# Kernel tuning notes

Hardware: AMD Instinct MI355X
Metric: run time of the kernel (lower is better)

## Reference

```python
import jax, jax.numpy as jnp
import numpy as np
from jax import lax

B, P, NB, NF, NC, R = 128, 2048, 2000, 250, 16, 128
LS = NB - NF  # number of simulated bins = len_bins_gensig - 1


def setup_inputs() -> dict:
    key = jax.random.key(0)
    ks = jax.random.split(key, 10)
    return {
        'batched_stim_spat': jax.random.normal(ks[0], (B, P), jnp.float32),
        'stim_time': jax.random.normal(ks[1], (NB,), jnp.float32),
        'batched_initial_spike_section': (jax.random.uniform(ks[2], (B, NF)) < 0.05).astype(jnp.float32),
        'batched_coupling_cells': (jax.random.uniform(ks[3], (B, NC, NB)) < 0.05).astype(jnp.float32),
        'spatial_filter': jax.random.normal(ks[4], (P,), jnp.float32) * 0.02,
        'spatial_bias': jnp.float32(-2.0),
        'stim_timecourse_filter': jax.random.normal(ks[5], (NF,), jnp.float32) * 0.1,
        'feedback_filter': jax.random.normal(ks[6], (NF,), jnp.float32) * 0.05 - 0.02,
        'coupling_filter': jax.random.normal(ks[7], (NC, NF), jnp.float32) * 0.05,
        'u': jax.random.uniform(ks[8], (LS, B, R), jnp.float32),
        'n_repeats': R,
    }


def _corr1d_valid(x, k):
    # torch F.conv1d is cross-correlation; lax conv is too (no kernel flip)
    # x: (n,), k: (m,) -> (n - m + 1,)
    out = lax.conv_general_dilated(x[None, None, :], k[None, None, :], (1,), 'VALID',
                                   dimension_numbers=('NCH', 'OIH', 'NCH'))
    return out[0, 0]


def reference(batched_stim_spat, stim_time, batched_initial_spike_section,
              batched_coupling_cells, spatial_filter, spatial_bias,
              stim_timecourse_filter, feedback_filter, coupling_filter, u, n_repeats):
    nf = stim_timecourse_filter.shape[0]

    # stimulus time component: (n_bins - nf + 1,)
    filt_time = _corr1d_valid(stim_time, stim_timecourse_filter)

    # spatial exp arg for separable linear-spatial GLM:
    # einsum('bpt,p->bt', stim_spat[:,:,None]*filt_time, spatial_filter)
    # factors into outer product of (stim_spat @ spatial_filter) and filt_time
    stim_gensig = (batched_stim_spat @ spatial_filter)[:, None] * filt_time[None, :] + spatial_bias  # (B, T)

    # coupling exp arg: conv1d over all coupled cells -> (B, T)
    coup = lax.conv_general_dilated(batched_coupling_cells, coupling_filter[None, :, :], (1,), 'VALID',
                                    dimension_numbers=('NCH', 'OIH', 'NCH'))[:, 0, :]

    gensig_piece = stim_gensig + coup  # (B, T) with T = n_bins - nf + 1
    len_sim = gensig_piece.shape[1] - 1

    # initial feedback window: last nf spike bins, broadcast over repeats
    batch = batched_stim_spat.shape[0]
    w0 = jnp.broadcast_to(batched_initial_spike_section[:, None, :], (batch, n_repeats, nf)) + 0.0

    def step(window, xs):
        g_t, u_t = xs  # (B,), (B, R)
        fb = jnp.einsum('brk,k->br', window, feedback_filter)
        g = g_t[:, None] + fb
        spike = (u_t < jax.nn.sigmoid(g)).astype(window.dtype)  # Bernoulli(sigmoid(g))
        window = jnp.concatenate([window[:, :, 1:], spike[:, :, None]], axis=2)
        return window, spike

    xs = (jnp.swapaxes(gensig_piece[:, :len_sim], 0, 1), u[:len_sim])  # ((LS,B), (LS,B,R))
    _, spikes = lax.scan(step, w0, xs)  # spikes: (LS, B, R)

    out = jnp.concatenate([w0, jnp.moveaxis(spikes, 0, 2)], axis=2)  # (B, R, n_bins)
    return out
```

## Files before the change

kernel.cpp:

```cpp
#include <hip/hip_runtime.h>
#include <math.h>

#define B_  128
#define P_  2048
#define NB_ 2000
#define NF_ 250
#define NC_ 16
#define R_  128
#define LS_ 1750
#define NT_ 1751
#define BR_ (B_ * R_)
#define H_  16
#define NBLK_ 110

typedef int v4i __attribute__((ext_vector_type(4)));

template <int CTRL>
__device__ __forceinline__ long long dpp64i(long long x) {
    int lo = (int)x, hi = (int)(x >> 32);
    lo = __builtin_amdgcn_mov_dpp(lo, CTRL, 0xF, 0xF, true);
    hi = __builtin_amdgcn_mov_dpp(hi, CTRL, 0xF, 0xF, true);
    return ((long long)(unsigned)lo) | ((long long)hi << 32);
}

__device__ __forceinline__ double logit_fast(float uf) {
    double u = (double)uf;
    double v = 1.0 - u;
    double qd = u / v;
    long long bits = __double_as_longlong(qd);
    int e = (int)((bits >> 52) & 0x7FF) - 1023;
    double m = __longlong_as_double((bits & 0xFFFFFFFFFFFFFLL) | 0x3FF0000000000000LL);
    if (m > 1.4142135623730951) { m *= 0.5; e += 1; }
    double s = (m - 1.0) / (m + 1.0);
    double z = s * s;
    double Q = fma(z, fma(z, fma(z, fma(z, fma(z, fma(z,
        0.06666666666666667, 0.07692307692307693), 0.09090909090909091),
        0.1111111111111111), 0.14285714285714285), 0.2), 0.3333333333333333);
    double logm = fma(2.0 * s, z * Q, 2.0 * s);
    return fma((double)e, 0.6931471805599453, logm);
}

__device__ __forceinline__ long long thrq_of(double lu, double fb) {
    double thr = lu - fb;
    thr = fmin(fmax(thr, -8.0), 8.0);
    double d = fma(thr, 0x1p45, 0x1.8p52);
    return (__double_as_longlong(d) & 0xFFFFFFFFFFFFFLL) - (1LL << 51);
}

__global__ __launch_bounds__(256) void k_pre(const float* __restrict__ st,
                                             const float* __restrict__ stf,
                                             const float* __restrict__ sp,
                                             const float* __restrict__ sf,
                                             double* __restrict__ ft,
                                             double* __restrict__ sdot) {
    if (blockIdx.x < 7) {
        int t = blockIdx.x * 256 + threadIdx.x;
        if (t >= NT_) return;
        double s = 0.0;
        for (int k = 0; k < NF_; ++k) s += (double)st[t + k] * (double)stf[k];
        ft[t] = s;
    } else {
        __shared__ double red[256];
        int b = blockIdx.x - 7;
        double s = 0.0;
        for (int p = threadIdx.x; p < P_; p += 256)
            s += (double)sp[(size_t)b * P_ + p] * (double)sf[p];
        red[threadIdx.x] = s;
        __syncthreads();
        for (int off = 128; off > 0; off >>= 1) {
            if (threadIdx.x < off) red[threadIdx.x] += red[threadIdx.x + off];
            __syncthreads();
        }
        if (threadIdx.x == 0) sdot[b] = red[0];
    }
}

__global__ __launch_bounds__(256) void k_coup(const float* __restrict__ cc,
                                              const float* __restrict__ cf,
                                              const double* __restrict__ sdot,
                                              const double* __restrict__ ft,
                                              const float* __restrict__ bias,
                                              double* __restrict__ gensig) {
    __shared__ __align__(16) float  ccs[NC_ * 512];
    __shared__ __align__(16) double cfs[NC_ * 256];
    __shared__ double red[3][64][4];
    int b = blockIdx.y, t0 = blockIdx.x * 256;
    int tid = threadIdx.x, lane = tid & 63, wv = tid >> 6;

    for (int idx = tid; idx < NC_ * 128; idx += 256) {
        int c = idx >> 7, j4 = (idx & 127) * 4, src = t0 + j4;
        const float* p = cc + ((size_t)b * NC_ + c) * NB_ + src;
        float4 v;
        if (src + 3 < NB_) v = *(const float4*)p;
        else {
            v.x = (src     < NB_) ? p[0] : 0.f;
            v.y = (src + 1 < NB_) ? p[1] : 0.f;
            v.z = (src + 2 < NB_) ? p[2] : 0.f;
            v.w = (src + 3 < NB_) ? p[3] : 0.f;
        }
        *(float4*)&ccs[c * 512 + j4] = v;
    }
    for (int idx = tid; idx < NC_ * 256; idx += 256) {
        int c = idx >> 8, k = idx & 255;
        cfs[idx] = (k < NF_) ? (double)cf[c * NF_ + k] : 0.0;
    }
    __syncthreads();

    double a0 = 0, a1 = 0, a2 = 0, a3 = 0;
    int base = lane * 4;
    for (int c = wv; c < NC_; c += 4) {
        const float*  row  = &ccs[c * 512];
        const double* crow = &cfs[c * 256];
        float4 cur = *(const float4*)&row[base];
        for (int k4 = 0; k4 < 252; k4 += 4) {
            float4 nxt = *(const float4*)&row[base + k4 + 4];
            double e0 = cur.x, e1 = cur.y, e2 = cur.z, e3 = cur.w;
            double e4 = nxt.x, e5 = nxt.y, e6 = nxt.z;
            double c0 = crow[k4], c1 = crow[k4 + 1], c2 = crow[k4 + 2], c3 = crow[k4 + 3];
            a0 += e0 * c0 + e1 * c1 + e2 * c2 + e3 * c3;
            a1 += e1 * c0 + e2 * c1 + e3 * c2 + e4 * c3;
            a2 += e2 * c0 + e3 * c1 + e4 * c2 + e5 * c3;
            a3 += e3 * c0 + e4 * c1 + e5 * c2 + e6 * c3;
            cur = nxt;
        }
    }
    if (wv > 0) {
        red[wv - 1][lane][0] = a0; red[wv - 1][lane][1] = a1;
        red[wv - 1][lane][2] = a2; red[wv - 1][lane][3] = a3;
    }
    __syncthreads();
    if (wv == 0) {
        a0 += red[0][lane][0] + red[1][lane][0] + red[2][lane][0];
        a1 += red[0][lane][1] + red[1][lane][1] + red[2][lane][1];
        a2 += red[0][lane][2] + red[1][lane][2] + red[2][lane][2];
        a3 += red[0][lane][3] + red[1][lane][3] + red[2][lane][3];
        double gb = (double)bias[0];
        double sd = sdot[b];
        double accs[4] = {a0, a1, a2, a3};
        int tb = t0 + base;
        for (int i = 0; i < 4; ++i) {
            int t = tb + i;
            if (t < LS_) gensig[(size_t)b * LS_ + t] = sd * ft[t] + gb + accs[i];
        }
    }
}

__global__ __launch_bounds__(512, 2) void k_scan(const double* __restrict__ gensig,
                                                 const float* __restrict__ u,
                                                 const float* __restrict__ iss,
                                                 const float* __restrict__ ff,
                                                 float* __restrict__ out) {
    __shared__ double farT_all[4][16 * 17];
    __shared__ double luring[2][4][4 * 64];
    int tid = threadIdx.x;
    int wv = tid >> 6, l = tid & 63;
    int swv = wv & 3;
    const bool isPrep = (wv >= 4);
    int gw = blockIdx.x * 4 + swv;
    int b = gw >> 3, rbase = (gw & 7) * 16;
    double* farT = &farT_all[swv][0];

    int lw = l & 15;
    int q  = l >> 4;
    int cn = l >> 2;
    int j  = l & 3;

    const double* gs   = gensig + (size_t)b * LS_;
    const float*  up   = u + b * R_ + rbase + cn;
    float*        op   = out + ((size_t)(b * R_ + rbase + cn)) * NB_ + NF_;
    const float*  issb = iss + b * NF_;

    unsigned long long W0 = 0, W1 = 0, W2 = 0, W3 = 0;
    v4i Bf[4][6];
    long long tq0 = 0, tq1 = 0, tq2 = 0, tq3 = 0;
    long long thrq0 = 0, thrq1 = 0, thrq2 = 0, thrq3 = 0;
    double gprep = 0.0;
    float ur0 = 0.f, ur1 = 0.f, ur2 = 0.f, ur3 = 0.f;

    if (!isPrep) {
        for (int idx = l; idx < 16 * NF_; idx += 64) {
            int c = idx / NF_, k = idx - c * NF_;
            out[((size_t)(b * R_ + rbase + c)) * NB_ + k] = issb[k];
        }
        for (int k = 0; k < NF_; ++k) {
            unsigned long long bit = (issb[k] > 0.5f) ? 1ull : 0ull;
            if      (k <  64) W0 |= bit << k;
            else if (k < 128) W1 |= bit << (k - 64);
            else if (k < 192) W2 |= bit << (k - 128);
            else              W3 |= bit << (k - 192);
        }
        int Bword[4][6][4];
#pragma unroll
        for (int kc = 0; kc < 4; ++kc)
#pragma unroll
            for (int p = 0; p < 6; ++p)
#pragma unroll
                for (int w = 0; w < 4; ++w) Bword[kc][p][w] = 0;
#pragma unroll
        for (int kc = 0; kc < 4; ++kc) {
#pragma unroll
            for (int jj = 0; jj < 16; ++jj) {
                int k = kc * 64 + q * 16 + jj;
                int idx = k - lw;
                long long v = 0;
                if (idx >= 0 && idx < NF_)
                    v = __double2ll_rn((double)ff[idx] * 281474976710656.0);
#pragma unroll
                for (int p = 0; p < 6; ++p) {
                    int d = (int)((v + 128) & 255) - 128;
                    v = (v - (long long)d) >> 8;
                    Bword[kc][p][jj >> 2] |= (d & 255) << ((jj & 3) * 8);
                }
            }
        }
#pragma unroll
        for (int kc = 0; kc < 4; ++kc)
#pragma unroll
            for (int p = 0; p < 6; ++p) {
                v4i t; t.x = Bword[kc][p][0]; t.y = Bword[kc][p][1];
                t.z = Bword[kc][p][2]; t.w = Bword[kc][p][3];
                Bf[kc][p] = t;
            }
        tq0 = __double2ll_rn((double)ff[249 - 4 * j] * 0x1p45);
        tq1 = __double2ll_rn((double)ff[248 - 4 * j] * 0x1p45);
        tq2 = __double2ll_rn((double)ff[247 - 4 * j] * 0x1p45);
        tq3 = __double2ll_rn((double)ff[246 - 4 * j] * 0x1p45);
    } else {
        ur0 = up[(size_t)(0  + j) * BR_];
        ur1 = up[(size_t)(4  + j) * BR_];
        ur2 = up[(size_t)(8  + j) * BR_];
        ur3 = up[(size_t)(12 + j) * BR_];
        luring[0][swv][  0 + l] = logit_fast(ur0);
        luring[0][swv][ 64 + l] = logit_fast(ur1);
        luring[0][swv][128 + l] = logit_fast(ur2);
        luring[0][swv][192 + l] = logit_fast(ur3);
        ur0 = up[(size_t)(16 + j) * BR_];
        ur1 = up[(size_t)(20 + j) * BR_];
        ur2 = up[(size_t)(24 + j) * BR_];
        ur3 = up[(size_t)(28 + j) * BR_];
        luring[1][swv][  0 + l] = logit_fast(ur0);
        luring[1][swv][ 64 + l] = logit_fast(ur1);
        luring[1][swv][128 + l] = logit_fast(ur2);
        luring[1][swv][192 + l] = logit_fast(ur3);
        ur0 = up[(size_t)(32 + j) * BR_];
        ur1 = up[(size_t)(36 + j) * BR_];
        ur2 = up[(size_t)(40 + j) * BR_];
        ur3 = up[(size_t)(44 + j) * BR_];
    }

    auto do_far = [&](double gp) {
        unsigned long long Sarr[4] = {W0, W1, W2, W3};
        v4i acc[6];
#pragma unroll
        for (int p = 0; p < 6; ++p) acc[p] = (v4i){0, 0, 0, 0};
#pragma unroll
        for (int kc = 0; kc < 4; ++kc) {
            unsigned f = (unsigned)((Sarr[kc] >> (q * 16)) & 0xFFFFull);
            v4i av;
            av.x = (int)((((f      ) & 0xFu) * 0x00204081u) & 0x01010101u);
            av.y = (int)((((f >>  4) & 0xFu) * 0x00204081u) & 0x01010101u);
            av.z = (int)((((f >>  8) & 0xFu) * 0x00204081u) & 0x01010101u);
            av.w = (int)((((f >> 12) & 0xFu) * 0x00204081u) & 0x01010101u);
#pragma unroll
            for (int p = 0; p < 6; ++p)
                acc[p] = __builtin_amdgcn_mfma_i32_16x16x64_i8(av, Bf[kc][p], acc[p], 0, 0, 0);
        }
#pragma unroll
        for (int r = 0; r < 4; ++r) {
            int lo = acc[0][r] + acc[1][r] * 256 + acc[2][r] * 65536;
            int hi = acc[3][r] + acc[4][r] * 256 + acc[5][r] * 65536;
            double fb = gp + (double)lo * 0x1p-48 + (double)hi * 0x1p-24;
            farT[(q * 4 + r) * 17 + lw] = fb;
        }
    };

    __syncthreads();

    if (!isPrep) {
        gprep = gs[lw];
        do_far(gprep);
        double lu0 = luring[0][swv][  0 + l];
        double lu1 = luring[0][swv][ 64 + l];
        double lu2 = luring[0][swv][128 + l];
        double lu3 = luring[0][swv][192 + l];
        __asm__ volatile("s_waitcnt lgkmcnt(0)" ::: "memory");
        thrq0 = thrq_of(lu0, farT[cn * 17 + j]);
        thrq1 = thrq_of(lu1, farT[cn * 17 + 4 + j]);
        thrq2 = thrq_of(lu2, farT[cn * 17 + 8 + j]);
        thrq3 = thrq_of(lu3, farT[cn * 17 + 12 + j]);
        { int tg = 16 + lw; if (tg > LS_ - 1) tg = LS_ - 1; gprep = gs[tg]; }
    }

    __syncthreads();

#define NSTEP(S, THRQ) { \
    long long thr = dpp64i<(S) * 0x55>(THRQ); \
    unsigned qb = (qreg >> (4 * j)) & 15u; \
    long long s = (((qb & 1u) ? tq0 : 0LL) + ((qb & 2u) ? tq1 : 0LL)) \
                + (((qb & 4u) ? tq2 : 0LL) + ((qb & 8u) ? tq3 : 0LL)); \
    s += dpp64i<0xB1>(s); \
    s += dpp64i<0x4E>(s); \
    bool sp = s > thr; \
    qreg = (qreg << 1) | (sp ? 1u : 0u); \
}

    int blk = 0;
    for (int t0 = 0; t0 < LS_; t0 += H_, ++blk) {
        if (!isPrep) {
            unsigned qreg = 0;
            NSTEP(0, thrq0) NSTEP(1, thrq0) NSTEP(2, thrq0) NSTEP(3, thrq0)
            NSTEP(0, thrq1) NSTEP(1, thrq1) NSTEP(2, thrq1) NSTEP(3, thrq1)
            NSTEP(0, thrq2) NSTEP(1, thrq2) NSTEP(2, thrq2) NSTEP(3, thrq2)
            NSTEP(0, thrq3) NSTEP(1, thrq3) NSTEP(2, thrq3) NSTEP(3, thrq3)

            unsigned q2 = (__brev(qreg) >> 16) & 0xFFFFu;
            int rem = LS_ - t0; if (rem > H_) rem = H_;
            int s0 = 4 * j;
            if (s0 + 3 < rem) {
                float4 o;
                o.x = (float)((q2 >> (s0    )) & 1u);
                o.y = (float)((q2 >> (s0 + 1)) & 1u);
                o.z = (float)((q2 >> (s0 + 2)) & 1u);
                o.w = (float)((q2 >> (s0 + 3)) & 1u);
                *(float4*)(op + t0 + s0) = o;
            } else {
#pragma unroll
                for (int e = 0; e < 4; ++e)
                    if (s0 + e < rem) op[t0 + s0 + e] = (float)((q2 >> (s0 + e)) & 1u);
            }

            if (t0 + H_ < LS_) {
                double lu0 = luring[(blk + 1) & 1][swv][  0 + l];
                double lu1 = luring[(blk + 1) & 1][swv][ 64 + l];
                double lu2 = luring[(blk + 1) & 1][swv][128 + l];
                double lu3 = luring[(blk + 1) & 1][swv][192 + l];

                int q2i = __builtin_amdgcn_ds_bpermute(lw << 4, (int)q2);
                unsigned long long q2n = (unsigned long long)(unsigned)q2i;
                W0 = (W0 >> 16) | (W1 << 48);
                W1 = (W1 >> 16) | (W2 << 48);
                W2 = (W2 >> 16) | (W3 << 48);
                W3 = (W3 >> 16) | (q2n << 42);

                do_far(gprep);
                __asm__ volatile("s_waitcnt lgkmcnt(0)" ::: "memory");
                thrq0 = thrq_of(lu0, farT[cn * 17 + j]);
                thrq1 = thrq_of(lu1, farT[cn * 17 + 4 + j]);
                thrq2 = thrq_of(lu2, farT[cn * 17 + 8 + j]);
                thrq3 = thrq_of(lu3, farT[cn * 17 + 12 + j]);

                int tg = t0 + 32 + lw; if (tg > LS_ - 1) tg = LS_ - 1;
                gprep = gs[tg];
            }
        } else {
            if (blk <= NBLK_ - 3) {
                double lu0 = logit_fast(ur0), lu1 = logit_fast(ur1);
                double lu2 = logit_fast(ur2), lu3 = logit_fast(ur3);
                luring[blk & 1][swv][  0 + l] = lu0;
                luring[blk & 1][swv][ 64 + l] = lu1;
                luring[blk & 1][swv][128 + l] = lu2;
                luring[blk & 1][swv][192 + l] = lu3;
                if (blk <= NBLK_ - 4) {
                    int T = (blk + 3) * H_;
                    int t_;
                    t_ = T + 0  + j; if (t_ > LS_ - 1) t_ = LS_ - 1; ur0 = up[(size_t)t_ * BR_];
                    t_ = T + 4  + j; if (t_ > LS_ - 1) t_ = LS_ - 1; ur1 = up[(size_t)t_ * BR_];
                    t_ = T + 8  + j; if (t_ > LS_ - 1) t_ = LS_ - 1; ur2 = up[(size_t)t_ * BR_];
                    t_ = T + 12 + j; if (t_ > LS_ - 1) t_ = LS_ - 1; ur3 = up[(size_t)t_ * BR_];
                }
            }
        }
        __syncthreads();
    }
#undef NSTEP
}

extern "C" void kernel_launch(void* const* d_in, const int* in_sizes, int n_in,
                              void* d_out, int out_size, void* d_ws, size_t ws_size,
                              hipStream_t stream) {
    const float* stim_spat = (const float*)d_in[0];
    const float* stim_time = (const float*)d_in[1];
    const float* iss       = (const float*)d_in[2];
    const float* cc        = (const float*)d_in[3];
    const float* sf        = (const float*)d_in[4];
    const float* bias      = (const float*)d_in[5];
    const float* stf       = (const float*)d_in[6];
    const float* ff        = (const float*)d_in[7];
    const float* cf        = (const float*)d_in[8];
    const float* u         = (const float*)d_in[9];
    (void)in_sizes; (void)n_in; (void)out_size; (void)ws_size;

    float* out = (float*)d_out;

    double* ws     = (double*)d_ws;
    double* gensig = ws;
    double* ft     = gensig + (size_t)B_ * LS_;
    double* sdot   = ft + NT_;

    k_pre  <<<135, 256, 0, stream>>>(stim_time, stf, stim_spat, sf, ft, sdot);
    k_coup <<<dim3(7, B_), 256, 0, stream>>>(cc, cf, sdot, ft, bias, gensig);
    k_scan <<<B_ * 2, 512, 0, stream>>>(gensig, u, iss, ff, out);
}
```

Baseline: 567.0 us.

## Replace per-step DPP reduction with per-lane forward-propagated threshold accumulators

Result: slower. 719.5 us (+26.9%).

```diff
diff --git a/kernel.cpp b/kernel.cpp
--- a/kernel.cpp
+++ b/kernel.cpp
@@ -172,8 +172,12 @@
 
     unsigned long long W0 = 0, W1 = 0, W2 = 0, W3 = 0;
     v4i Bf[4][6];
-    long long tq0 = 0, tq1 = 0, tq2 = 0, tq3 = 0;
-    long long thrq0 = 0, thrq1 = 0, thrq2 = 0, thrq3 = 0;
+    long long acc[16];
+#pragma unroll
+    for (int k = 0; k < 16; ++k) acc[k] = 0;
+    long long tqs[15];
+#pragma unroll
+    for (int k = 0; k < 15; ++k) tqs[k] = 0;
     double gprep = 0.0;
     float ur0 = 0.f, ur1 = 0.f, ur2 = 0.f, ur3 = 0.f;
 
@@ -221,38 +225,41 @@
                 t.z = Bword[kc][p][2]; t.w = Bword[kc][p][3];
                 Bf[kc][p] = t;
             }
-        tq0 = __double2ll_rn((double)ff[249 - 4 * j] * 0x1p45);
-        tq1 = __double2ll_rn((double)ff[248 - 4 * j] * 0x1p45);
-        tq2 = __double2ll_rn((double)ff[247 - 4 * j] * 0x1p45);
-        tq3 = __double2ll_rn((double)ff[246 - 4 * j] * 0x1p45);
+#pragma unroll
+        for (int i = 0; i < 15; ++i) {
+            long long v = __double2ll_rn((double)ff[249 - i] * 0x1p45);
+            int lo = __builtin_amdgcn_readfirstlane((int)v);
+            int hi = __builtin_amdgcn_readfirstlane((int)(v >> 32));
+            tqs[i] = ((long long)(unsigned)lo) | ((long long)hi << 32);
+        }
     } else {
-        ur0 = up[(size_t)(0  + j) * BR_];
-        ur1 = up[(size_t)(4  + j) * BR_];
-        ur2 = up[(size_t)(8  + j) * BR_];
-        ur3 = up[(size_t)(12 + j) * BR_];
+        ur0 = up[(size_t)(4 * j + 0) * BR_];
+        ur1 = up[(size_t)(4 * j + 1) * BR_];
+        ur2 = up[(size_t)(4 * j + 2) * BR_];
+        ur3 = up[(size_t)(4 * j + 3) * BR_];
         luring[0][swv][  0 + l] = logit_fast(ur0);
         luring[0][swv][ 64 + l] = logit_fast(ur1);
         luring[0][swv][128 + l] = logit_fast(ur2);
         luring[0][swv][192 + l] = logit_fast(ur3);
-        ur0 = up[(size_t)(16 + j) * BR_];
-        ur1 = up[(size_t)(20 + j) * BR_];
-        ur2 = up[(size_t)(24 + j) * BR_];
-        ur3 = up[(size_t)(28 + j) * BR_];
+        ur0 = up[(size_t)(16 + 4 * j + 0) * BR_];
+        ur1 = up[(size_t)(16 + 4 * j + 1) * BR_];
+        ur2 = up[(size_t)(16 + 4 * j + 2) * BR_];
+        ur3 = up[(size_t)(16 + 4 * j + 3) * BR_];
         luring[1][swv][  0 + l] = logit_fast(ur0);
         luring[1][swv][ 64 + l] = logit_fast(ur1);
         luring[1][swv][128 + l] = logit_fast(ur2);
         luring[1][swv][192 + l] = logit_fast(ur3);
-        ur0 = up[(size_t)(32 + j) * BR_];
-        ur1 = up[(size_t)(36 + j) * BR_];
-        ur2 = up[(size_t)(40 + j) * BR_];
-        ur3 = up[(size_t)(44 + j) * BR_];
+        ur0 = up[(size_t)(32 + 4 * j + 0) * BR_];
+        ur1 = up[(size_t)(32 + 4 * j + 1) * BR_];
+        ur2 = up[(size_t)(32 + 4 * j + 2) * BR_];
+        ur3 = up[(size_t)(32 + 4 * j + 3) * BR_];
     }
 
     auto do_far = [&](double gp) {
         unsigned long long Sarr[4] = {W0, W1, W2, W3};
-        v4i acc[6];
-#pragma unroll
-        for (int p = 0; p < 6; ++p) acc[p] = (v4i){0, 0, 0, 0};
+        v4i accm[6];
+#pragma unroll
+        for (int p = 0; p < 6; ++p) accm[p] = (v4i){0, 0, 0, 0};
 #pragma unroll
         for (int kc = 0; kc < 4; ++kc) {
             unsigned f = (unsigned)((Sarr[kc] >> (q * 16)) & 0xFFFFull);
@@ -263,16 +270,31 @@
             av.w = (int)((((f >> 12) & 0xFu) * 0x00204081u) & 0x01010101u);
 #pragma unroll
             for (int p = 0; p < 6; ++p)
-                acc[p] = __builtin_amdgcn_mfma_i32_16x16x64_i8(av, Bf[kc][p], acc[p], 0, 0, 0);
+                accm[p] = __builtin_amdgcn_mfma_i32_16x16x64_i8(av, Bf[kc][p], accm[p], 0, 0, 0);
         }
 #pragma unroll
         for (int r = 0; r < 4; ++r) {
-            int lo = acc[0][r] + acc[1][r] * 256 + acc[2][r] * 65536;
-            int hi = acc[3][r] + acc[4][r] * 256 + acc[5][r] * 65536;
+            int lo = accm[0][r] + accm[1][r] * 256 + accm[2][r] * 65536;
+            int hi = accm[3][r] + accm[4][r] * 256 + accm[5][r] * 65536;
             double fb = gp + (double)lo * 0x1p-48 + (double)hi * 0x1p-24;
             farT[(q * 4 + r) * 17 + lw] = fb;
         }
     };
+
+#define ACC_INIT(LU0, LU1, LU2, LU3) { \
+    long long own0 = -thrq_of(LU0, farT[cn * 17 + 4 * j + 0]); \
+    long long own1 = -thrq_of(LU1, farT[cn * 17 + 4 * j + 1]); \
+    long long own2 = -thrq_of(LU2, farT[cn * 17 + 4 * j + 2]); \
+    long long own3 = -thrq_of(LU3, farT[cn * 17 + 4 * j + 3]); \
+    acc[ 0] = dpp64i<0x00>(own0); acc[ 1] = dpp64i<0x00>(own1); \
+    acc[ 2] = dpp64i<0x00>(own2); acc[ 3] = dpp64i<0x00>(own3); \
+    acc[ 4] = dpp64i<0x55>(own0); acc[ 5] = dpp64i<0x55>(own1); \
+    acc[ 6] = dpp64i<0x55>(own2); acc[ 7] = dpp64i<0x55>(own3); \
+    acc[ 8] = dpp64i<0xAA>(own0); acc[ 9] = dpp64i<0xAA>(own1); \
+    acc[10] = dpp64i<0xAA>(own2); acc[11] = dpp64i<0xAA>(own3); \
+    acc[12] = dpp64i<0xFF>(own0); acc[13] = dpp64i<0xFF>(own1); \
+    acc[14] = dpp64i<0xFF>(own2); acc[15] = dpp64i<0xFF>(own3); \
+}
 
     __syncthreads();
 
@@ -284,36 +306,26 @@
         double lu2 = luring[0][swv][128 + l];
         double lu3 = luring[0][swv][192 + l];
         __asm__ volatile("s_waitcnt lgkmcnt(0)" ::: "memory");
-        thrq0 = thrq_of(lu0, farT[cn * 17 + j]);
-        thrq1 = thrq_of(lu1, farT[cn * 17 + 4 + j]);
-        thrq2 = thrq_of(lu2, farT[cn * 17 + 8 + j]);
-        thrq3 = thrq_of(lu3, farT[cn * 17 + 12 + j]);
+        ACC_INIT(lu0, lu1, lu2, lu3)
         { int tg = 16 + lw; if (tg > LS_ - 1) tg = LS_ - 1; gprep = gs[tg]; }
     }
 
     __syncthreads();
-
-#define NSTEP(S, THRQ) { \
-    long long thr = dpp64i<(S) * 0x55>(THRQ); \
-    unsigned qb = (qreg >> (4 * j)) & 15u; \
-    long long s = (((qb & 1u) ? tq0 : 0LL) + ((qb & 2u) ? tq1 : 0LL)) \
-                + (((qb & 4u) ? tq2 : 0LL) + ((qb & 8u) ? tq3 : 0LL)); \
-    s += dpp64i<0xB1>(s); \
-    s += dpp64i<0x4E>(s); \
-    bool sp = s > thr; \
-    qreg = (qreg << 1) | (sp ? 1u : 0u); \
-}
 
     int blk = 0;
     for (int t0 = 0; t0 < LS_; t0 += H_, ++blk) {
         if (!isPrep) {
             unsigned qreg = 0;
-            NSTEP(0, thrq0) NSTEP(1, thrq0) NSTEP(2, thrq0) NSTEP(3, thrq0)
-            NSTEP(0, thrq1) NSTEP(1, thrq1) NSTEP(2, thrq1) NSTEP(3, thrq1)
-            NSTEP(0, thrq2) NSTEP(1, thrq2) NSTEP(2, thrq2) NSTEP(3, thrq2)
-            NSTEP(0, thrq3) NSTEP(1, thrq3) NSTEP(2, thrq3) NSTEP(3, thrq3)
-
-            unsigned q2 = (__brev(qreg) >> 16) & 0xFFFFu;
+#pragma unroll
+            for (int t = 0; t < 16; ++t) {
+                bool sp = acc[t] > 0;
+                qreg |= (sp ? (1u << t) : 0u);
+#pragma unroll
+                for (int k = t + 1; k < 16; ++k)
+                    acc[k] += sp ? tqs[k - t - 1] : 0LL;
+            }
+            unsigned q2 = qreg;
+
             int rem = LS_ - t0; if (rem > H_) rem = H_;
             int s0 = 4 * j;
             if (s0 + 3 < rem) {
@@ -344,10 +356,7 @@
 
                 do_far(gprep);
                 __asm__ volatile("s_waitcnt lgkmcnt(0)" ::: "memory");
-                thrq0 = thrq_of(lu0, farT[cn * 17 + j]);
-                thrq1 = thrq_of(lu1, farT[cn * 17 + 4 + j]);
-                thrq2 = thrq_of(lu2, farT[cn * 17 + 8 + j]);
-                thrq3 = thrq_of(lu3, farT[cn * 17 + 12 + j]);
+                ACC_INIT(lu0, lu1, lu2, lu3)
 
                 int tg = t0 + 32 + lw; if (tg > LS_ - 1) tg = LS_ - 1;
                 gprep = gs[tg];
@@ -363,16 +372,18 @@
                 if (blk <= NBLK_ - 4) {
                     int T = (blk + 3) * H_;
                     int t_;
-                    t_ = T + 0  + j; if (t_ > LS_ - 1) t_ = LS_ - 1; ur0 = up[(size_t)t_ * BR_];
-                    t_ = T + 4  + j; if (t_ > LS_ - 1) t_ = LS_ - 1; ur1 = up[(size_t)t_ * BR_];
-                    t_ = T + 8  + j; if (t_ > LS_ - 1) t_ = LS_ - 1; ur2 = up[(size_t)t_ * BR_];
-                    t_ = T + 12 + j; if (t_ > LS_ - 1) t_ = LS_ - 1; ur3 = up[(size_t)t_ * BR_];
+                    t_ = T + 4 * j + 0; if (t_ > LS_ - 1) t_ = LS_ - 1; ur0 = up[(size_t)t_ * BR_];
+                    t_ = T + 4 * j + 1; if (t_ > LS_ - 1) t_ = LS_ - 1; ur1 = up[(size_t)t_ * BR_];
+                    t_ = T + 4 * j + 2; if (t_ > LS_ - 1) t_ = LS_ - 1; ur2 = up[(size_t)t_ * BR_];
+                    t_ = T + 4 * j + 3; if (t_ > LS_ - 1) t_ = LS_ - 1; ur3 = up[(size_t)t_ * BR_];
                 }
             }
         }
         __syncthreads();
     }
-#undef NSTEP
+#undef ACC_INIT
+
+    (void)lw;
 }
 
 extern "C" void kernel_launch(void* const* d_in, const int* in_sizes, int n_in,
```

## Replace fixed-point DPP step reduction with double-precision ballot-based speculative spike step

Applied to the files above, without the earlier changes.

After: 562.7 us. No clear change (-0.7%).

```diff
diff --git a/kernel.cpp b/kernel.cpp
--- a/kernel.cpp
+++ b/kernel.cpp
@@ -15,36 +15,52 @@
 
 typedef int v4i __attribute__((ext_vector_type(4)));
 
-template <int CTRL>
-__device__ __forceinline__ long long dpp64i(long long x) {
-    int lo = (int)x, hi = (int)(x >> 32);
-    lo = __builtin_amdgcn_mov_dpp(lo, CTRL, 0xF, 0xF, true);
-    hi = __builtin_amdgcn_mov_dpp(hi, CTRL, 0xF, 0xF, true);
-    return ((long long)(unsigned)lo) | ((long long)hi << 32);
+__device__ __forceinline__ unsigned csel32(unsigned a, unsigned b, unsigned long long m) {
+    unsigned r;
+    asm("v_cndmask_b32 %0, %1, %2, %3" : "=v"(r) : "v"(a), "v"(b), "s"(m));
+    return r;
+}
+
+__device__ __forceinline__ double dsel2(double t, unsigned long long m) {
+    long long tb = __double_as_longlong(t);
+    int tlo = (int)tb, thi = (int)(tb >> 32);
+    int rlo, rhi;
+    asm("v_cndmask_b32 %0, 0, %2, %4\n\t"
+        "v_cndmask_b32 %1, 0, %3, %4"
+        : "=&v"(rlo), "=&v"(rhi)
+        : "v"(tlo), "v"(thi), "s"(m));
+    return __longlong_as_double(((long long)(unsigned)rlo) | ((long long)rhi << 32));
+}
+
+__device__ __forceinline__ double dand(double t, int m) {
+    return __longlong_as_double(__double_as_longlong(t) & (long long)m);
+}
+
+__device__ __forceinline__ double fdiv_fast(double a, double b) {
+    double r;
+    asm("v_rcp_f64 %0, %1" : "=v"(r) : "v"(b));
+    r = fma(fma(-b, r, 1.0), r, r);
+    r = fma(fma(-b, r, 1.0), r, r);
+    double q = a * r;
+    q = fma(fma(-b, q, a), r, q);
+    return q;
 }
 
 __device__ __forceinline__ double logit_fast(float uf) {
     double u = (double)uf;
     double v = 1.0 - u;
-    double qd = u / v;
+    double qd = fdiv_fast(u, v);
     long long bits = __double_as_longlong(qd);
     int e = (int)((bits >> 52) & 0x7FF) - 1023;
     double m = __longlong_as_double((bits & 0xFFFFFFFFFFFFFLL) | 0x3FF0000000000000LL);
     if (m > 1.4142135623730951) { m *= 0.5; e += 1; }
-    double s = (m - 1.0) / (m + 1.0);
+    double s = fdiv_fast(m - 1.0, m + 1.0);
     double z = s * s;
-    double Q = fma(z, fma(z, fma(z, fma(z, fma(z, fma(z,
-        0.06666666666666667, 0.07692307692307693), 0.09090909090909091),
-        0.1111111111111111), 0.14285714285714285), 0.2), 0.3333333333333333);
+    double Q = fma(z, fma(z, fma(z, fma(z,
+        0.09090909090909091, 0.1111111111111111),
+        0.14285714285714285), 0.2), 0.3333333333333333);
     double logm = fma(2.0 * s, z * Q, 2.0 * s);
     return fma((double)e, 0.6931471805599453, logm);
-}
-
-__device__ __forceinline__ long long thrq_of(double lu, double fb) {
-    double thr = lu - fb;
-    thr = fmin(fmax(thr, -8.0), 8.0);
-    double d = fma(thr, 0x1p45, 0x1.8p52);
-    return (__double_as_longlong(d) & 0xFFFFFFFFFFFFFLL) - (1LL << 51);
 }
 
 __global__ __launch_bounds__(256) void k_pre(const float* __restrict__ st,
@@ -164,6 +180,7 @@
     int q  = l >> 4;
     int cn = l >> 2;
     int j  = l & 3;
+    int jo = 16 + j;
 
     const double* gs   = gensig + (size_t)b * LS_;
     const float*  up   = u + b * R_ + rbase + cn;
@@ -172,8 +189,10 @@
 
     unsigned long long W0 = 0, W1 = 0, W2 = 0, W3 = 0;
     v4i Bf[4][6];
-    long long tq0 = 0, tq1 = 0, tq2 = 0, tq3 = 0;
-    long long thrq0 = 0, thrq1 = 0, thrq2 = 0, thrq3 = 0;
+    double T1d = 0, T2d = 0, T3d = 0, T4d = 0, T5d = 0, T6d = 0;
+    double tp7 = 0, tp8 = 0, tp9 = 0, tp10 = 0, tp11 = 0, tp12 = 0, tp13 = 0, tp14 = 0;
+    double tp15 = 0;
+    double thr0 = 0, thr1 = 0, thr2 = 0, thr3 = 0;
     double gprep = 0.0;
     float ur0 = 0.f, ur1 = 0.f, ur2 = 0.f, ur3 = 0.f;
 
@@ -221,10 +240,11 @@
                 t.z = Bword[kc][p][2]; t.w = Bword[kc][p][3];
                 Bf[kc][p] = t;
             }
-        tq0 = __double2ll_rn((double)ff[249 - 4 * j] * 0x1p45);
-        tq1 = __double2ll_rn((double)ff[248 - 4 * j] * 0x1p45);
-        tq2 = __double2ll_rn((double)ff[247 - 4 * j] * 0x1p45);
-        tq3 = __double2ll_rn((double)ff[246 - 4 * j] * 0x1p45);
+        T1d  = (double)ff[249]; T2d  = (double)ff[248]; T3d  = (double)ff[247];
+        T4d  = (double)ff[246]; T5d  = (double)ff[245]; T6d  = (double)ff[244];
+        tp7  = (double)ff[243]; tp8  = (double)ff[242]; tp9  = (double)ff[241];
+        tp10 = (double)ff[240]; tp11 = (double)ff[239]; tp12 = (double)ff[238];
+        tp13 = (double)ff[237]; tp14 = (double)ff[236]; tp15 = (double)ff[235];
     } else {
         ur0 = up[(size_t)(0  + j) * BR_];
         ur1 = up[(size_t)(4  + j) * BR_];
@@ -250,9 +270,9 @@
 
     auto do_far = [&](double gp) {
         unsigned long long Sarr[4] = {W0, W1, W2, W3};
-        v4i acc[6];
-#pragma unroll
-        for (int p = 0; p < 6; ++p) acc[p] = (v4i){0, 0, 0, 0};
+        v4i accm[6];
+#pragma unroll
+        for (int p = 0; p < 6; ++p) accm[p] = (v4i){0, 0, 0, 0};
 #pragma unroll
         for (int kc = 0; kc < 4; ++kc) {
             unsigned f = (unsigned)((Sarr[kc] >> (q * 16)) & 0xFFFFull);
@@ -263,15 +283,28 @@
             av.w = (int)((((f >> 12) & 0xFu) * 0x00204081u) & 0x01010101u);
 #pragma unroll
             for (int p = 0; p < 6; ++p)
-                acc[p] = __builtin_amdgcn_mfma_i32_16x16x64_i8(av, Bf[kc][p], acc[p], 0, 0, 0);
+                accm[p] = __builtin_amdgcn_mfma_i32_16x16x64_i8(av, Bf[kc][p], accm[p], 0, 0, 0);
         }
 #pragma unroll
         for (int r = 0; r < 4; ++r) {
-            int lo = acc[0][r] + acc[1][r] * 256 + acc[2][r] * 65536;
-            int hi = acc[3][r] + acc[4][r] * 256 + acc[5][r] * 65536;
+            int lo = accm[0][r] + accm[1][r] * 256 + accm[2][r] * 65536;
+            int hi = accm[3][r] + accm[4][r] * 256 + accm[5][r] * 65536;
             double fb = gp + (double)lo * 0x1p-48 + (double)hi * 0x1p-24;
             farT[(q * 4 + r) * 17 + lw] = fb;
         }
+    };
+
+    auto xbcalc = [&](int e4, unsigned qsnap) -> double {
+        unsigned qs = qsnap >> e4;
+        double x = (dand(tp7,  __builtin_amdgcn_sbfe((int)qs, jo - 7,  1)) +
+                    dand(tp8,  __builtin_amdgcn_sbfe((int)qs, jo - 8,  1))) +
+                   (dand(tp9,  __builtin_amdgcn_sbfe((int)qs, jo - 9,  1)) +
+                    dand(tp10, __builtin_amdgcn_sbfe((int)qs, jo - 10, 1)));
+        double y = (dand(tp11, __builtin_amdgcn_sbfe((int)qs, jo - 11, 1)) +
+                    dand(tp12, __builtin_amdgcn_sbfe((int)qs, jo - 12, 1))) +
+                   (dand(tp13, __builtin_amdgcn_sbfe((int)qs, jo - 13, 1)) +
+                    dand(tp14, __builtin_amdgcn_sbfe((int)qs, jo - 14, 1)));
+        return (x + y) + dand(tp15, __builtin_amdgcn_sbfe((int)qs, jo - 15, 1));
     };
 
     __syncthreads();
@@ -284,36 +317,58 @@
         double lu2 = luring[0][swv][128 + l];
         double lu3 = luring[0][swv][192 + l];
         __asm__ volatile("s_waitcnt lgkmcnt(0)" ::: "memory");
-        thrq0 = thrq_of(lu0, farT[cn * 17 + j]);
-        thrq1 = thrq_of(lu1, farT[cn * 17 + 4 + j]);
-        thrq2 = thrq_of(lu2, farT[cn * 17 + 8 + j]);
-        thrq3 = thrq_of(lu3, farT[cn * 17 + 12 + j]);
+        thr0 = lu0 - farT[cn * 17 +  0 + j];
+        thr1 = lu1 - farT[cn * 17 +  4 + j];
+        thr2 = lu2 - farT[cn * 17 +  8 + j];
+        thr3 = lu3 - farT[cn * 17 + 12 + j];
         { int tg = 16 + lw; if (tg > LS_ - 1) tg = LS_ - 1; gprep = gs[tg]; }
     }
 
     __syncthreads();
 
-#define NSTEP(S, THRQ) { \
-    long long thr = dpp64i<(S) * 0x55>(THRQ); \
-    unsigned qb = (qreg >> (4 * j)) & 15u; \
-    long long s = (((qb & 1u) ? tq0 : 0LL) + ((qb & 2u) ? tq1 : 0LL)) \
-                + (((qb & 4u) ? tq2 : 0LL) + ((qb & 8u) ? tq3 : 0LL)); \
-    s += dpp64i<0xB1>(s); \
-    s += dpp64i<0x4E>(s); \
-    bool sp = s > thr; \
-    qreg = (qreg << 1) | (sp ? 1u : 0u); \
+#define STEP(T, XB, THR) { \
+    double s23 = dsel2(T2d, sp2) + dsel2(T3d, sp3); \
+    double s456 = dsel2(T4d, sp4) + (dsel2(T5d, sp5) + dsel2(T6d, sp6)); \
+    double X = (XB) + (s23 + s456); \
+    double Y = X + T1d; \
+    unsigned long long Bm0 = __ballot(X > (THR)); \
+    unsigned long long Bm1 = __ballot(Y > (THR)); \
+    unsigned long long b0n = (Bm0 >> ((T) & 3)) & QP; \
+    unsigned long long b1n = (Bm1 >> ((T) & 3)) & QP; \
+    unsigned long long sn = b0n ^ (sp1 & (b1n ^ b0n)); \
+    unsigned long long fl = sn | (sn << 1); fl |= (fl << 2); \
+    sp6 = sp5; sp5 = sp4; sp4 = sp3; sp3 = sp2; sp2 = sp1; sp1 = fl; \
+    QL = csel32(QL, QL | (1u << (16 + (T))), fl); \
 }
 
     int blk = 0;
     for (int t0 = 0; t0 < LS_; t0 += H_, ++blk) {
         if (!isPrep) {
-            unsigned qreg = 0;
-            NSTEP(0, thrq0) NSTEP(1, thrq0) NSTEP(2, thrq0) NSTEP(3, thrq0)
-            NSTEP(0, thrq1) NSTEP(1, thrq1) NSTEP(2, thrq1) NSTEP(3, thrq1)
-            NSTEP(0, thrq2) NSTEP(1, thrq2) NSTEP(2, thrq2) NSTEP(3, thrq2)
-            NSTEP(0, thrq3) NSTEP(1, thrq3) NSTEP(2, thrq3) NSTEP(3, thrq3)
-
-            unsigned q2 = (__brev(qreg) >> 16) & 0xFFFFu;
+            const unsigned long long QP = 0x1111111111111111ull;
+            unsigned QL = 0;
+            unsigned long long sp1 = 0, sp2 = 0, sp3 = 0, sp4 = 0, sp5 = 0, sp6 = 0;
+            double XB0 = 0.0, XB1, XB2, XB3;
+            STEP(0, XB0, thr0)
+            { unsigned qs1 = QL; XB1 = xbcalc(4, qs1); }
+            STEP(1, XB0, thr0)
+            STEP(2, XB0, thr0)
+            STEP(3, XB0, thr0)
+            STEP(4, XB1, thr1)
+            { unsigned qs2 = QL; XB2 = xbcalc(8, qs2); }
+            STEP(5, XB1, thr1)
+            STEP(6, XB1, thr1)
+            STEP(7, XB1, thr1)
+            STEP(8, XB2, thr2)
+            { unsigned qs3 = QL; XB3 = xbcalc(12, qs3); }
+            STEP(9,  XB2, thr2)
+            STEP(10, XB2, thr2)
+            STEP(11, XB2, thr2)
+            STEP(12, XB3, thr3)
+            STEP(13, XB3, thr3)
+            STEP(14, XB3, thr3)
+            STEP(15, XB3, thr3)
+            unsigned q2 = QL >> 16;
+
             int rem = LS_ - t0; if (rem > H_) rem = H_;
             int s0 = 4 * j;
             if (s0 + 3 < rem) {
@@ -344,10 +399,10 @@
 
                 do_far(gprep);
                 __asm__ volatile("s_waitcnt lgkmcnt(0)" ::: "memory");
-                thrq0 = thrq_of(lu0, farT[cn * 17 + j]);
-                thrq1 = thrq_of(lu1, farT[cn * 17 + 4 + j]);
-                thrq2 = thrq_of(lu2, farT[cn * 17 + 8 + j]);
-                thrq3 = thrq_of(lu3, farT[cn * 17 + 12 + j]);
+                thr0 = lu0 - farT[cn * 17 +  0 + j];
+                thr1 = lu1 - farT[cn * 17 +  4 + j];
+                thr2 = lu2 - farT[cn * 17 +  8 + j];
+                thr3 = lu3 - farT[cn * 17 + 12 + j];
 
                 int tg = t0 + 32 + lw; if (tg > LS_ - 1) tg = LS_ - 1;
                 gprep = gs[tg];
@@ -363,16 +418,16 @@
                 if (blk <= NBLK_ - 4) {
                     int T = (blk + 3) * H_;
                     int t_;
-                    t_ = T + 0  + j; if (t_ > LS_ - 1) t_ = LS_ - 1; ur0 = up[(size_t)t_ * BR_];
-                    t_ = T + 4  + j; if (t_ > LS_ - 1) t_ = LS_ - 1; ur1 = up[(size_t)t_ * BR_];
-                    t_ = T + 8  + j; if (t_ > LS_ - 1) t_ = LS_ - 1; ur2 = up[(size_t)t_ * BR_];
+                    t_ = T +  0 + j; if (t_ > LS_ - 1) t_ = LS_ - 1; ur0 = up[(size_t)t_ * BR_];
+                    t_ = T +  4 + j; if (t_ > LS_ - 1) t_ = LS_ - 1; ur1 = up[(size_t)t_ * BR_];
+                    t_ = T +  8 + j; if (t_ > LS_ - 1) t_ = LS_ - 1; ur2 = up[(size_t)t_ * BR_];
                     t_ = T + 12 + j; if (t_ > LS_ - 1) t_ = LS_ - 1; ur3 = up[(size_t)t_ * BR_];
                 }
             }
         }
         __syncthreads();
     }
-#undef NSTEP
+#undef STEP
 }
 
 extern "C" void kernel_launch(void* const* d_in, const int* in_sizes, int n_in,
```
